# Kernel optimization log

Measured on AMD Instinct MI355X. Metric: run time of the kernel, lower is better.

Reference implementation:

```python
import jax, jax.numpy as jnp
import numpy as np

N_NODES = 100000
N_EDGES = 600000
N_GRAPHS = 512


def _glorot(key, shape):
    fan_in, fan_out = shape
    lim = np.sqrt(6.0 / (fan_in + fan_out)).astype(np.float32)
    return jax.random.uniform(key, shape, jnp.float32, -lim, lim)


def setup_inputs() -> dict:
    key = jax.random.key(0)
    ks = jax.random.split(key, 12)
    x = jax.random.normal(ks[0], (N_NODES, 3), jnp.float32)
    edge_index = jax.random.randint(ks[1], (2, N_EDGES), 0, N_NODES, jnp.int64)
    batch = jnp.sort(jax.random.randint(ks[2], (N_NODES,), 0, N_GRAPHS, jnp.int64))
    return {
        "x": x,
        "edge_index": edge_index,
        "batch": batch,
        "W1": _glorot(ks[3], (3, 128)),   "b1": jnp.zeros((128,), jnp.float32),
        "W2": _glorot(ks[4], (128, 128)), "b2": jnp.zeros((128,), jnp.float32),
        "W3": _glorot(ks[5], (128, 64)),  "b3": jnp.zeros((64,), jnp.float32),
        "Wl": _glorot(ks[6], (64, 1)),    "bl": jnp.zeros((1,), jnp.float32),
    }


def _gcn_conv(h, W, b, src, dst, deg_inv_sqrt):
    # linear transform, then normalized gather-scatter aggregation (self-loops
    # already included in src/dst and deg_inv_sqrt).
    h = h @ W                                            # [N, F_out]
    norm = deg_inv_sqrt[src] * deg_inv_sqrt[dst]         # [E+N]
    msg = h[src] * norm[:, None]                         # [E+N, F_out]
    out = jax.ops.segment_sum(msg, dst, num_segments=N_NODES)
    return out + b


def reference(x, edge_index, batch, W1, b1, W2, b2, W3, b3, Wl, bl):
    # add self-loops (GCNConv default add_self_loops=True)
    loop = jnp.arange(N_NODES, dtype=edge_index.dtype)
    src = jnp.concatenate([edge_index[0], loop])
    dst = jnp.concatenate([edge_index[1], loop])
    # symmetric normalization deg^{-1/2} (in-degree at target, edge weight 1)
    deg = jax.ops.segment_sum(jnp.ones_like(dst, jnp.float32), dst,
                              num_segments=N_NODES)
    deg_inv_sqrt = jnp.where(deg > 0, jax.lax.rsqrt(jnp.maximum(deg, 1.0)), 0.0)

    h = jax.nn.relu(_gcn_conv(x, W1, b1, src, dst, deg_inv_sqrt))
    h = jax.nn.relu(_gcn_conv(h, W2, b2, src, dst, deg_inv_sqrt))
    h = jax.nn.relu(_gcn_conv(h, W3, b3, src, dst, deg_inv_sqrt))

    # global mean pool over graphs
    sums = jax.ops.segment_sum(h, batch, num_segments=N_GRAPHS)    # [G, 64]
    counts = jax.ops.segment_sum(jnp.ones((N_NODES,), jnp.float32), batch,
                                 num_segments=N_GRAPHS)
    pooled = sums / jnp.maximum(counts, 1.0)[:, None]

    return pooled @ Wl + bl                                        # [G, 1]
```

## Files before the change

### kernel.cpp

```cpp
#include <hip/hip_runtime.h>

#define N_NODES 100000
#define N_EDGES 600000
#define N_GRAPHS 512
#define BSTRIDE 32

typedef __attribute__((ext_vector_type(8))) short short8;
typedef __attribute__((ext_vector_type(4))) float floatx4;
typedef __attribute__((ext_vector_type(2))) float floatx2;

__device__ __forceinline__ unsigned short f2bf(float f) {
    unsigned int u = __float_as_uint(f);
    u += 0x7FFFu + ((u >> 16) & 1u);
    return (unsigned short)(u >> 16);
}
__device__ __forceinline__ short8 pack8s(const float* a, float s) {
    short8 r;
    #pragma unroll
    for (int j = 0; j < 8; ++j) r[j] = (short)f2bf(a[j] * s);
    return r;
}

__device__ __forceinline__ uint2 pack_fp8x8(const float* v) {
    uint2 r;
    unsigned int a = 0;
    a = __builtin_amdgcn_cvt_pk_fp8_f32(v[0], v[1], a, 0);
    a = __builtin_amdgcn_cvt_pk_fp8_f32(v[2], v[3], a, 1);
    unsigned int b = 0;
    b = __builtin_amdgcn_cvt_pk_fp8_f32(v[4], v[5], b, 0);
    b = __builtin_amdgcn_cvt_pk_fp8_f32(v[6], v[7], b, 1);
    r.x = a; r.y = b;
    return r;
}
__device__ __forceinline__ unsigned char f2fp8(float v) {
    return (unsigned char)(__builtin_amdgcn_cvt_pk_fp8_f32(v, v, 0u, 0) & 0xFFu);
}
__device__ __forceinline__ void fma4_fp8(float* a, unsigned int w, float n) {
    floatx2 p;
    p = __builtin_amdgcn_cvt_pk_f32_fp8(w, 0); a[0] = fmaf(p[0], n, a[0]); a[1] = fmaf(p[1], n, a[1]);
    p = __builtin_amdgcn_cvt_pk_f32_fp8(w, 1); a[2] = fmaf(p[0], n, a[2]); a[3] = fmaf(p[1], n, a[3]);
}
__device__ __forceinline__ void init4_fp8(float* a, unsigned int w) {
    floatx2 p;
    p = __builtin_amdgcn_cvt_pk_f32_fp8(w, 0); a[0] = p[0]; a[1] = p[1];
    p = __builtin_amdgcn_cvt_pk_f32_fp8(w, 1); a[2] = p[0]; a[3] = p[1];
}
__device__ __forceinline__ void fma16_fp8(float* a, uint4 v, float n) {
    fma4_fp8(a +  0, v.x, n); fma4_fp8(a +  4, v.y, n);
    fma4_fp8(a +  8, v.z, n); fma4_fp8(a + 12, v.w, n);
}
__device__ __forceinline__ void init16_fp8(float* a, uint4 v) {
    init4_fp8(a +  0, v.x); init4_fp8(a +  4, v.y);
    init4_fp8(a +  8, v.z); init4_fp8(a + 12, v.w);
}

__device__ __forceinline__ void pack_one(const float* __restrict__ W, unsigned short* __restrict__ out,
                                         int idx, int N) {
    int lane = idx & 63;
    int ks = (idx >> 6) & 3;
    int ct = idx >> 8;
    int n = ct * 16 + (lane & 15);
    int kbase = ks * 32 + (lane >> 4) * 8;
    #pragma unroll
    for (int j = 0; j < 8; ++j)
        out[(size_t)idx * 8 + j] = f2bf(W[(size_t)(kbase + j) * N + n]);
}

#define NB_E ((N_EDGES + 255) / 256)
__global__ void k_build_pack(const int* __restrict__ src, const int* __restrict__ dst,
                             int* __restrict__ deg, int* __restrict__ bsrc,
                             const float* __restrict__ W2, const float* __restrict__ W3,
                             unsigned short* __restrict__ Wp2, unsigned short* __restrict__ Wp3) {
    if (blockIdx.x >= NB_E) {
        int idx = (blockIdx.x - NB_E) * 256 + threadIdx.x;
        if (idx < 2048) pack_one(W2, Wp2, idx, 128);
        else if (idx < 3072) pack_one(W3, Wp3, idx - 2048, 64);
        return;
    }
    int e = blockIdx.x * 256 + threadIdx.x;
    if (e >= N_EDGES) return;
    int d = dst[e];
    int slot = atomicAdd(&deg[d], 1);
    if (slot < BSTRIDE) bsrc[d * BSTRIDE + slot] = src[e];
}

#define NB1 6250
__global__ __launch_bounds__(256) void k_node1(const float* __restrict__ x,
                                               const int* __restrict__ deg,
                                               const int* __restrict__ bsrc,
                                               const float* __restrict__ W1,
                                               const float* __restrict__ b1,
                                               unsigned char* __restrict__ out) {
    int tid = threadIdx.x;
    __shared__ float Ws[384];
    __shared__ float bs[128];
    for (int i = tid; i < 384; i += 256) Ws[i] = W1[i];
    if (tid < 128) bs[tid] = b1[tid];
    __syncthreads();
    int gw = (blockIdx.x * 256 + tid) >> 6;
    int lane = tid & 63;
    int sub = lane >> 4, l16 = lane & 15;
    int node = gw * 4 + sub;
    int dgn = deg[node];
    int dgb = dgn < BSTRIDE ? dgn : BSTRIDE;
    float dnode = rsqrtf((float)(dgn + 1));
    int b0 = node * BSTRIDE;
    float p0 = 0.f, p1 = 0.f, p2 = 0.f;
    for (int u = l16; u < dgb; u += 16) {
        int s = bsrc[b0 + u];
        float n = rsqrtf((float)(deg[s] + 1)) * dnode;
        p0 = fmaf(x[s * 3 + 0], n, p0);
        p1 = fmaf(x[s * 3 + 1], n, p1);
        p2 = fmaf(x[s * 3 + 2], n, p2);
    }
    #pragma unroll
    for (int m = 8; m > 0; m >>= 1) {
        p0 += __shfl_xor(p0, m, 64);
        p1 += __shfl_xor(p1, m, 64);
        p2 += __shfl_xor(p2, m, 64);
    }
    float s2 = dnode * dnode;
    float a0 = fmaf(x[node * 3 + 0], s2, p0);
    float a1 = fmaf(x[node * 3 + 1], s2, p1);
    float a2 = fmaf(x[node * 3 + 2], s2, p2);
    int f = l16 * 8;
    float v[8];
    #pragma unroll
    for (int j = 0; j < 8; ++j)
        v[j] = fmaxf(bs[f + j] + a0 * Ws[f + j] + a1 * Ws[128 + f + j] + a2 * Ws[256 + f + j], 0.f)
               * dnode;
    *(uint2*)(out + (size_t)node * 128 + f) = pack_fp8x8(v);
}

__global__ __launch_bounds__(256) void k_layer23(const unsigned char* __restrict__ h1,
                                                 const int* __restrict__ deg,
                                                 const int* __restrict__ bsrc,
                                                 const unsigned short* __restrict__ Wp2,
                                                 const float* __restrict__ b2,
                                                 const unsigned short* __restrict__ Wp3,
                                                 unsigned char* __restrict__ Q2f8) {
    __shared__ unsigned short Asb[32][136];
    __shared__ unsigned short Hsb[32][136];
    __shared__ float disS[32];
    int tid = threadIdx.x;
    int wave = tid >> 6, lane = tid & 63;
    int quad = lane >> 4, m16 = lane & 15;
    int base = blockIdx.x * 32;

    {
        int sub = lane >> 3, l8 = lane & 7;
        int r = wave * 8 + sub;
        int node = base + r;
        int dgn = deg[node];
        int dgb = dgn < BSTRIDE ? dgn : BSTRIDE;
        float dnode = rsqrtf((float)(dgn + 1));
        if (l8 == 0) disS[r] = dnode;
        const int* bp = bsrc + node * BSTRIDE;
        uint4 i0 = *(const uint4*)(bp);
        uint4 i1 = *(const uint4*)(bp + 4);
        int idx[8] = {(int)i0.x, (int)i0.y, (int)i0.z, (int)i0.w,
                      (int)i1.x, (int)i1.y, (int)i1.z, (int)i1.w};
        float nn[8];
        #pragma unroll
        for (int u = 0; u < 8; ++u) {
            bool val = (u < dgb) && ((unsigned)idx[u] < N_NODES);
            if (!val) idx[u] = node;
            nn[u] = (u < dgb) ? 1.0f : 0.0f;
        }
        uint4 self = *(const uint4*)(h1 + (size_t)node * 128 + l8 * 16);
        uint4 g[8];
        #pragma unroll
        for (int u = 0; u < 8; ++u)
            g[u] = *(const uint4*)(h1 + (size_t)idx[u] * 128 + l8 * 16);
        float a[16];
        init16_fp8(a, self);
        #pragma unroll
        for (int u = 0; u < 8; ++u) fma16_fp8(a, g[u], nn[u]);
        for (int eb = 8; eb < dgb; eb += 8) {
            int idx2[8]; float nn2[8];
            #pragma unroll
            for (int u = 0; u < 8; ++u) {
                int uu = eb + u;
                int s = bsrc[bp - bsrc + (uu < dgb ? uu : 0)];
                if ((unsigned)s >= N_NODES) s = node;
                idx2[u] = s;
                nn2[u] = (uu < dgb) ? 1.0f : 0.0f;
            }
            uint4 g2[8];
            #pragma unroll
            for (int u = 0; u < 8; ++u)
                g2[u] = *(const uint4*)(h1 + (size_t)idx2[u] * 128 + l8 * 16);
            #pragma unroll
            for (int u = 0; u < 8; ++u) fma16_fp8(a, g2[u], nn2[u]);
        }
        *(short8*)(&Asb[r][l8 * 16])     = pack8s(a, dnode);
        *(short8*)(&Asb[r][l8 * 16 + 8]) = pack8s(a + 8, dnode);
    }
    __syncthreads();

    int mt = wave & 1;
    int ch = wave >> 1;
    {
        short8 af[4];
        #pragma unroll
        for (int ks = 0; ks < 4; ++ks)
            af[ks] = *(const short8*)(&Asb[mt * 16 + m16][ks * 32 + quad * 8]);
        floatx4 acc[4];
        #pragma unroll
        for (int ct = 0; ct < 4; ++ct) acc[ct] = (floatx4){0.f, 0.f, 0.f, 0.f};
        #pragma unroll
        for (int ct = 0; ct < 4; ++ct) {
            int gct = ch * 4 + ct;
            #pragma unroll
            for (int ks = 0; ks < 4; ++ks) {
                short8 bf = *(const short8*)(Wp2 + ((size_t)(gct * 4 + ks) * 64 + lane) * 8);
                acc[ct] = __builtin_amdgcn_mfma_f32_16x16x32_bf16(af[ks], bf, acc[ct], 0, 0, 0);
            }
        }
        #pragma unroll
        for (int ct = 0; ct < 4; ++ct) {
            int col = (ch * 4 + ct) * 16 + m16;
            float bv = b2[col];
            #pragma unroll
            for (int r = 0; r < 4; ++r) {
                int row = mt * 16 + quad * 4 + r;
                Hsb[row][col] = f2bf(fmaxf(acc[ct][r] + bv, 0.0f));
            }
        }
    }
    __syncthreads();

    {
        int cp = wave >> 1;
        short8 hf[4];
        #pragma unroll
        for (int ks = 0; ks < 4; ++ks)
            hf[ks] = *(const short8*)(&Hsb[mt * 16 + m16][ks * 32 + quad * 8]);
        floatx4 acc3[2];
        acc3[0] = (floatx4){0.f, 0.f, 0.f, 0.f};
        acc3[1] = (floatx4){0.f, 0.f, 0.f, 0.f};
        #pragma unroll
        for (int ct = 0; ct < 2; ++ct) {
            int gct = cp * 2 + ct;
            #pragma unroll
            for (int ks = 0; ks < 4; ++ks) {
                short8 bf = *(const short8*)(Wp3 + ((size_t)(gct * 4 + ks) * 64 + lane) * 8);
                acc3[ct] = __builtin_amdgcn_mfma_f32_16x16x32_bf16(hf[ks], bf, acc3[ct], 0, 0, 0);
            }
        }
        #pragma unroll
        for (int ct = 0; ct < 2; ++ct) {
            int col = (cp * 2 + ct) * 16 + m16;
            #pragma unroll
            for (int r = 0; r < 4; ++r) {
                int rr = mt * 16 + quad * 4 + r;
                long row = base + rr;
                Q2f8[row * 64 + col] = f2fp8(acc3[ct][r] * disS[rr]);
            }
        }
    }
}

__global__ __launch_bounds__(256) void k_agg64_dot(const unsigned char* __restrict__ h,
                                                   const int* __restrict__ deg,
                                                   const int* __restrict__ bsrc,
                                                   const float* __restrict__ bias,
                                                   const float* __restrict__ Wl,
                                                   float* __restrict__ s_out) {
    int gw = (blockIdx.x * 256 + threadIdx.x) >> 6;
    if (gw >= N_NODES / 16) return;
    int lane = threadIdx.x & 63;
    int sub = lane >> 2, l4 = lane & 3;
    int node = gw * 16 + sub;
    int dgn = deg[node];
    int dgb = dgn < BSTRIDE ? dgn : BSTRIDE;
    float dnode = rsqrtf((float)(dgn + 1));
    const int* bp = bsrc + node * BSTRIDE;
    uint4 i0 = *(const uint4*)(bp);
    uint4 i1 = *(const uint4*)(bp + 4);
    int idx[8] = {(int)i0.x, (int)i0.y, (int)i0.z, (int)i0.w,
                  (int)i1.x, (int)i1.y, (int)i1.z, (int)i1.w};
    float nn[8];
    #pragma unroll
    for (int u = 0; u < 8; ++u) {
        bool val = (u < dgb) && ((unsigned)idx[u] < N_NODES);
        if (!val) idx[u] = node;
        nn[u] = (u < dgb) ? 1.0f : 0.0f;
    }
    uint4 self = *(const uint4*)(h + (size_t)node * 64 + l4 * 16);
    uint4 g[8];
    #pragma unroll
    for (int u = 0; u < 8; ++u)
        g[u] = *(const uint4*)(h + (size_t)idx[u] * 64 + l4 * 16);
    float a[16];
    init16_fp8(a, self);
    #pragma unroll
    for (int u = 0; u < 8; ++u) fma16_fp8(a, g[u], nn[u]);
    for (int eb = 8; eb < dgb; eb += 8) {
        int idx2[8]; float nn2[8];
        #pragma unroll
        for (int u = 0; u < 8; ++u) {
            int uu = eb + u;
            int s = bp[uu < dgb ? uu : 0];
            if ((unsigned)s >= N_NODES) s = node;
            idx2[u] = s;
            nn2[u] = (uu < dgb) ? 1.0f : 0.0f;
        }
        uint4 g2[8];
        #pragma unroll
        for (int u = 0; u < 8; ++u)
            g2[u] = *(const uint4*)(h + (size_t)idx2[u] * 64 + l4 * 16);
        #pragma unroll
        for (int u = 0; u < 8; ++u) fma16_fp8(a, g2[u], nn2[u]);
    }
    int f = l4 * 16;
    float v = 0.f;
    #pragma unroll
    for (int j = 0; j < 16; ++j)
        v = fmaf(fmaxf(fmaf(a[j], dnode, bias[f + j]), 0.f), Wl[f + j], v);
    v += __shfl_xor(v, 1, 64);
    v += __shfl_xor(v, 2, 64);
    if (l4 == 0) s_out[node] = v;
}

__global__ __launch_bounds__(256) void k_pool2(const float* __restrict__ s,
                                               const int* __restrict__ batch,
                                               const float* __restrict__ bl,
                                               float* __restrict__ out) {
    int g = blockIdx.x;
    int tid = threadIdx.x;
    int lo = 0, hi = N_NODES;
    while (lo < hi) { int m = (lo + hi) >> 1; if (batch[m] < g) lo = m + 1; else hi = m; }
    int lo2 = lo, hi2 = N_NODES;
    while (lo2 < hi2) { int m = (lo2 + hi2) >> 1; if (batch[m] < g + 1) lo2 = m + 1; else hi2 = m; }
    float acc = 0.0f;
    for (int n = lo + tid; n < lo2; n += 256) acc += s[n];
    __shared__ float sm[256];
    sm[tid] = acc; __syncthreads();
    for (int off = 128; off > 0; off >>= 1) {
        if (tid < off) sm[tid] += sm[tid + off];
        __syncthreads();
    }
    if (tid == 0) out[g] = sm[0] / fmaxf((float)(lo2 - lo), 1.0f) + bl[0];
}

extern "C" void kernel_launch(void* const* d_in, const int* in_sizes, int n_in,
                              void* d_out, int out_size, void* d_ws, size_t ws_size,
                              hipStream_t stream) {
    const float* x     = (const float*)d_in[0];
    const int*   ei    = (const int*)d_in[1];
    const int*   batch = (const int*)d_in[2];
    const float* W1 = (const float*)d_in[3];
    const float* b1 = (const float*)d_in[4];
    const float* W2 = (const float*)d_in[5];
    const float* b2 = (const float*)d_in[6];
    const float* W3 = (const float*)d_in[7];
    const float* b3 = (const float*)d_in[8];
    const float* Wl = (const float*)d_in[9];
    const float* bl = (const float*)d_in[10];
    float* out = (float*)d_out;

    const int* e_src = ei;
    const int* e_dst = ei + N_EDGES;

    char* ws = (char*)d_ws;
    size_t off = 0;
    auto alloc = [&](size_t bytes) -> char* {
        char* p = ws + off;
        off = (off + bytes + 255) & ~(size_t)255;
        return p;
    };
    int*   deg   = (int*)  alloc((size_t)N_NODES * 4);
    int*   bsrc  = (int*)  alloc((size_t)N_NODES * BSTRIDE * 4);
    float* nscal = (float*)alloc((size_t)N_NODES * 4);
    unsigned char*  P1f8 = (unsigned char*) alloc((size_t)N_NODES * 128);
    unsigned char*  Q2f8 = (unsigned char*) alloc((size_t)N_NODES * 64);
    unsigned short* Wp2  = (unsigned short*)alloc((size_t)128 * 128 * 2);
    unsigned short* Wp3  = (unsigned short*)alloc((size_t)128 * 64 * 2);

    hipMemsetAsync(deg, 0, (size_t)N_NODES * 4, stream);

    k_build_pack<<<NB_E + 12, 256, 0, stream>>>(e_src, e_dst, deg, bsrc, W2, W3, Wp2, Wp3);

    k_node1<<<NB1, 256, 0, stream>>>(x, deg, bsrc, W1, b1, P1f8);

    k_layer23<<<N_NODES / 32, 256, 0, stream>>>(P1f8, deg, bsrc, Wp2, b2, Wp3, Q2f8);

    k_agg64_dot<<<(N_NODES / 16 + 3) / 4, 256, 0, stream>>>(Q2f8, deg, bsrc, b3, Wl, nscal);

    k_pool2<<<N_GRAPHS, 256, 0, stream>>>(nscal, batch, bl, out);
}
```

Measured before the change: 176.1 us.

## Fuse graph mean-pool partial sums into final aggregation kernel via shared atomics

The final 64-wide aggregation kernel now also does the graph pooling. Each block accumulates per-node scalars into a shared-memory per-graph buffer and flushes it to a global per-graph sum with atomics, which removes the per-node scalar array and the 512-block reduction kernel. A small one-block kernel divides by the counts and adds the bias. The overflow neighbor loops in both aggregation kernels now load indices as vectors instead of one scalar at a time. The cost is float atomics, which make the summation order nondeterministic, plus a larger memset that also zeroes the graph sums.

```diff
diff --git a/kernel.cpp b/kernel.cpp
--- a/kernel.cpp
+++ b/kernel.cpp
@@ -177,13 +177,16 @@
         #pragma unroll
         for (int u = 0; u < 8; ++u) fma16_fp8(a, g[u], nn[u]);
         for (int eb = 8; eb < dgb; eb += 8) {
-            int idx2[8]; float nn2[8];
+            uint4 j0 = *(const uint4*)(bp + eb);
+            uint4 j1 = *(const uint4*)(bp + eb + 4);
+            int idx2[8] = {(int)j0.x, (int)j0.y, (int)j0.z, (int)j0.w,
+                           (int)j1.x, (int)j1.y, (int)j1.z, (int)j1.w};
+            float nn2[8];
             #pragma unroll
             for (int u = 0; u < 8; ++u) {
                 int uu = eb + u;
-                int s = bsrc[bp - bsrc + (uu < dgb ? uu : 0)];
-                if ((unsigned)s >= N_NODES) s = node;
-                idx2[u] = s;
+                bool val = (uu < dgb) && ((unsigned)idx2[u] < N_NODES);
+                if (!val) idx2[u] = node;
                 nn2[u] = (uu < dgb) ? 1.0f : 0.0f;
             }
             uint4 g2[8];
@@ -261,87 +264,104 @@
     }
 }
 
-__global__ __launch_bounds__(256) void k_agg64_dot(const unsigned char* __restrict__ h,
-                                                   const int* __restrict__ deg,
-                                                   const int* __restrict__ bsrc,
-                                                   const float* __restrict__ bias,
-                                                   const float* __restrict__ Wl,
-                                                   float* __restrict__ s_out) {
-    int gw = (blockIdx.x * 256 + threadIdx.x) >> 6;
-    if (gw >= N_NODES / 16) return;
-    int lane = threadIdx.x & 63;
+__global__ __launch_bounds__(256) void k_agg64_pool(const unsigned char* __restrict__ h,
+                                                    const int* __restrict__ deg,
+                                                    const int* __restrict__ bsrc,
+                                                    const float* __restrict__ bias,
+                                                    const float* __restrict__ Wl,
+                                                    const int* __restrict__ batch,
+                                                    float* __restrict__ gsum) {
+    __shared__ float sp[68];
+    __shared__ int gminS;
+    int tid = threadIdx.x;
+    int gw = blockIdx.x * 4 + (tid >> 6);
+    int lane = tid & 63;
     int sub = lane >> 2, l4 = lane & 3;
-    int node = gw * 16 + sub;
-    int dgn = deg[node];
-    int dgb = dgn < BSTRIDE ? dgn : BSTRIDE;
-    float dnode = rsqrtf((float)(dgn + 1));
-    const int* bp = bsrc + node * BSTRIDE;
-    uint4 i0 = *(const uint4*)(bp);
-    uint4 i1 = *(const uint4*)(bp + 4);
-    int idx[8] = {(int)i0.x, (int)i0.y, (int)i0.z, (int)i0.w,
-                  (int)i1.x, (int)i1.y, (int)i1.z, (int)i1.w};
-    float nn[8];
-    #pragma unroll
-    for (int u = 0; u < 8; ++u) {
-        bool val = (u < dgb) && ((unsigned)idx[u] < N_NODES);
-        if (!val) idx[u] = node;
-        nn[u] = (u < dgb) ? 1.0f : 0.0f;
-    }
-    uint4 self = *(const uint4*)(h + (size_t)node * 64 + l4 * 16);
-    uint4 g[8];
-    #pragma unroll
-    for (int u = 0; u < 8; ++u)
-        g[u] = *(const uint4*)(h + (size_t)idx[u] * 64 + l4 * 16);
-    float a[16];
-    init16_fp8(a, self);
-    #pragma unroll
-    for (int u = 0; u < 8; ++u) fma16_fp8(a, g[u], nn[u]);
-    for (int eb = 8; eb < dgb; eb += 8) {
-        int idx2[8]; float nn2[8];
+    bool valid = gw < N_NODES / 16;
+    int node = valid ? gw * 16 + sub : 0;
+    if (tid == 0) gminS = batch[blockIdx.x * 64];
+    for (int i = tid; i < 68; i += 256) sp[i] = 0.0f;
+    __syncthreads();
+
+    float v = 0.f;
+    if (valid) {
+        int dgn = deg[node];
+        int dgb = dgn < BSTRIDE ? dgn : BSTRIDE;
+        float dnode = rsqrtf((float)(dgn + 1));
+        const int* bp = bsrc + node * BSTRIDE;
+        uint4 i0 = *(const uint4*)(bp);
+        uint4 i1 = *(const uint4*)(bp + 4);
+        int idx[8] = {(int)i0.x, (int)i0.y, (int)i0.z, (int)i0.w,
+                      (int)i1.x, (int)i1.y, (int)i1.z, (int)i1.w};
+        float nn[8];
         #pragma unroll
         for (int u = 0; u < 8; ++u) {
-            int uu = eb + u;
-            int s = bp[uu < dgb ? uu : 0];
-            if ((unsigned)s >= N_NODES) s = node;
-            idx2[u] = s;
-            nn2[u] = (uu < dgb) ? 1.0f : 0.0f;
-        }
-        uint4 g2[8];
+            bool val = (u < dgb) && ((unsigned)idx[u] < N_NODES);
+            if (!val) idx[u] = node;
+            nn[u] = (u < dgb) ? 1.0f : 0.0f;
+        }
+        uint4 self = *(const uint4*)(h + (size_t)node * 64 + l4 * 16);
+        uint4 g[8];
         #pragma unroll
         for (int u = 0; u < 8; ++u)
-            g2[u] = *(const uint4*)(h + (size_t)idx2[u] * 64 + l4 * 16);
-        #pragma unroll
-        for (int u = 0; u < 8; ++u) fma16_fp8(a, g2[u], nn2[u]);
-    }
-    int f = l4 * 16;
-    float v = 0.f;
-    #pragma unroll
-    for (int j = 0; j < 16; ++j)
-        v = fmaf(fmaxf(fmaf(a[j], dnode, bias[f + j]), 0.f), Wl[f + j], v);
-    v += __shfl_xor(v, 1, 64);
-    v += __shfl_xor(v, 2, 64);
-    if (l4 == 0) s_out[node] = v;
-}
-
-__global__ __launch_bounds__(256) void k_pool2(const float* __restrict__ s,
-                                               const int* __restrict__ batch,
-                                               const float* __restrict__ bl,
-                                               float* __restrict__ out) {
-    int g = blockIdx.x;
-    int tid = threadIdx.x;
+            g[u] = *(const uint4*)(h + (size_t)idx[u] * 64 + l4 * 16);
+        float a[16];
+        init16_fp8(a, self);
+        #pragma unroll
+        for (int u = 0; u < 8; ++u) fma16_fp8(a, g[u], nn[u]);
+        for (int eb = 8; eb < dgb; eb += 8) {
+            uint4 j0 = *(const uint4*)(bp + eb);
+            uint4 j1 = *(const uint4*)(bp + eb + 4);
+            int idx2[8] = {(int)j0.x, (int)j0.y, (int)j0.z, (int)j0.w,
+                           (int)j1.x, (int)j1.y, (int)j1.z, (int)j1.w};
+            float nn2[8];
+            #pragma unroll
+            for (int u = 0; u < 8; ++u) {
+                int uu = eb + u;
+                bool val = (uu < dgb) && ((unsigned)idx2[u] < N_NODES);
+                if (!val) idx2[u] = node;
+                nn2[u] = (uu < dgb) ? 1.0f : 0.0f;
+            }
+            uint4 g2[8];
+            #pragma unroll
+            for (int u = 0; u < 8; ++u)
+                g2[u] = *(const uint4*)(h + (size_t)idx2[u] * 64 + l4 * 16);
+            #pragma unroll
+            for (int u = 0; u < 8; ++u) fma16_fp8(a, g2[u], nn2[u]);
+        }
+        int f = l4 * 16;
+        #pragma unroll
+        for (int j = 0; j < 16; ++j)
+            v = fmaf(fmaxf(fmaf(a[j], dnode, bias[f + j]), 0.f), Wl[f + j], v);
+        v += __shfl_xor(v, 1, 64);
+        v += __shfl_xor(v, 2, 64);
+    }
+
+    if (valid && l4 == 0) {
+        int gi = batch[node] - gminS;
+        if (gi < 68) atomicAdd(&sp[gi], v);
+        else         atomicAdd(&gsum[batch[node]], v);
+    }
+    __syncthreads();
+    int lastn = blockIdx.x * 64 + 63; if (lastn >= N_NODES) lastn = N_NODES - 1;
+    int span = batch[lastn] - gminS + 1;
+    if (span > 68) span = 68;
+    if (tid < span) {
+        float p = sp[tid];
+        if (p != 0.0f) atomicAdd(&gsum[gminS + tid], p);
+    }
+}
+
+__global__ void k_poolfin(const float* __restrict__ gsum,
+                          const int* __restrict__ batch,
+                          const float* __restrict__ bl,
+                          float* __restrict__ out) {
+    int g = threadIdx.x;
     int lo = 0, hi = N_NODES;
     while (lo < hi) { int m = (lo + hi) >> 1; if (batch[m] < g) lo = m + 1; else hi = m; }
     int lo2 = lo, hi2 = N_NODES;
     while (lo2 < hi2) { int m = (lo2 + hi2) >> 1; if (batch[m] < g + 1) lo2 = m + 1; else hi2 = m; }
-    float acc = 0.0f;
-    for (int n = lo + tid; n < lo2; n += 256) acc += s[n];
-    __shared__ float sm[256];
-    sm[tid] = acc; __syncthreads();
-    for (int off = 128; off > 0; off >>= 1) {
-        if (tid < off) sm[tid] += sm[tid + off];
-        __syncthreads();
-    }
-    if (tid == 0) out[g] = sm[0] / fmaxf((float)(lo2 - lo), 1.0f) + bl[0];
+    out[g] = gsum[g] / fmaxf((float)(lo2 - lo), 1.0f) + bl[0];
 }
 
 extern "C" void kernel_launch(void* const* d_in, const int* in_sizes, int n_in,
@@ -371,14 +391,14 @@
         return p;
     };
     int*   deg   = (int*)  alloc((size_t)N_NODES * 4);
+    float* gsum  = (float*)alloc((size_t)N_GRAPHS * 4);
     int*   bsrc  = (int*)  alloc((size_t)N_NODES * BSTRIDE * 4);
-    float* nscal = (float*)alloc((size_t)N_NODES * 4);
     unsigned char*  P1f8 = (unsigned char*) alloc((size_t)N_NODES * 128);
     unsigned char*  Q2f8 = (unsigned char*) alloc((size_t)N_NODES * 64);
     unsigned short* Wp2  = (unsigned short*)alloc((size_t)128 * 128 * 2);
     unsigned short* Wp3  = (unsigned short*)alloc((size_t)128 * 64 * 2);
 
-    hipMemsetAsync(deg, 0, (size_t)N_NODES * 4, stream);
+    hipMemsetAsync(deg, 0, (size_t)((char*)gsum - (char*)deg) + (size_t)N_GRAPHS * 4, stream);
 
     k_build_pack<<<NB_E + 12, 256, 0, stream>>>(e_src, e_dst, deg, bsrc, W2, W3, Wp2, Wp3);
 
@@ -386,7 +406,7 @@
 
     k_layer23<<<N_NODES / 32, 256, 0, stream>>>(P1f8, deg, bsrc, Wp2, b2, Wp3, Q2f8);
 
-    k_agg64_dot<<<(N_NODES / 16 + 3) / 4, 256, 0, stream>>>(Q2f8, deg, bsrc, b3, Wl, nscal);
-
-    k_pool2<<<N_GRAPHS, 256, 0, stream>>>(nscal, batch, bl, out);
-}
+    k_agg64_pool<<<(N_NODES / 16 + 3) / 4, 256, 0, stream>>>(Q2f8, deg, bsrc, b3, Wl, batch, gsum);
+
+    k_poolfin<<<1, N_GRAPHS, 0, stream>>>(gsum, batch, bl, out);
+}
```

New measurement: 181.6 us. 1.03x slower.
